# Performance work log

Hardware: AMD Instinct MI355X
Metric: run time of the kernel (lower is better)

Reference implementation:

```python
import jax, jax.numpy as jnp
import numpy as np

EPS = 1e-12

def _l2n(v):
    return v / (jnp.linalg.norm(v) + EPS)

def _sn(w, u, v):
    """One power iteration of spectral norm. w: [out, in] (1x1 conv flattened).
    u, v updates carry no gradient (requires_grad=False in torch); sigma grads flow through w."""
    v1 = jax.lax.stop_gradient(_l2n(w.T @ u))
    u1 = jax.lax.stop_gradient(_l2n(w @ v1))
    sigma = u1 @ (w @ v1)
    return w / sigma

def setup_inputs() -> dict:
    key = jax.random.key(0)
    ks = jax.random.split(key, 16)
    B, C, H, W = 4, 64, 64, 64
    d_qk, d_v = C // 8, C // 2
    inp = {
        "x": jax.random.normal(ks[0], (B, C, H, W), dtype=jnp.float32),
        "w_theta": jax.random.normal(ks[1], (d_qk, C), dtype=jnp.float32) * 0.05,
        "w_phi": jax.random.normal(ks[2], (d_qk, C), dtype=jnp.float32) * 0.05,
        "w_g": jax.random.normal(ks[3], (d_v, C), dtype=jnp.float32) * 0.05,
        "w_o": jax.random.normal(ks[4], (C, d_v), dtype=jnp.float32) * 0.05,
        "gamma": jax.random.normal(ks[5], (1,), dtype=jnp.float32),
        "u_theta": _l2n(jax.random.normal(ks[6], (d_qk,), dtype=jnp.float32)),
        "v_theta": _l2n(jax.random.normal(ks[7], (C,), dtype=jnp.float32)),
        "u_phi": _l2n(jax.random.normal(ks[8], (d_qk,), dtype=jnp.float32)),
        "v_phi": _l2n(jax.random.normal(ks[9], (C,), dtype=jnp.float32)),
        "u_g": _l2n(jax.random.normal(ks[10], (d_v,), dtype=jnp.float32)),
        "v_g": _l2n(jax.random.normal(ks[11], (C,), dtype=jnp.float32)),
        "u_o": _l2n(jax.random.normal(ks[12], (C,), dtype=jnp.float32)),
        "v_o": _l2n(jax.random.normal(ks[13], (d_v,), dtype=jnp.float32)),
    }
    return inp

def reference(x, w_theta, w_phi, w_g, w_o, gamma,
              u_theta, v_theta, u_phi, v_phi, u_g, v_g, u_o, v_o):
    B, C, H, W = x.shape
    HW = H * W
    wt = _sn(w_theta, u_theta, v_theta)
    wp = _sn(w_phi, u_phi, v_phi)
    wg = _sn(w_g, u_g, v_g)
    wo = _sn(w_o, u_o, v_o)
    xf = x.reshape(B, C, HW)                      # [B, C, N]
    theta = jnp.einsum('oc,bcn->bon', wt, xf)     # [B, C/8, N]
    phi = jnp.einsum('oc,bcn->bon', wp, xf)       # [B, C/8, N]
    g = jnp.einsum('oc,bcn->bon', wg, xf)         # [B, C/2, N]
    scores = jnp.einsum('bci,bcj->bij', theta, phi)  # [B, N, N]
    beta = jax.nn.softmax(scores, axis=1)            # softmax over dim=1 (rows), as in torch code
    o = jnp.einsum('bci,bij->bcj', g, beta)          # [B, C/2, N]
    out = jnp.einsum('oc,bcn->bon', wo, o).reshape(B, C, H, W)
    return gamma.reshape(()) * out + x
```

## Files before the change

kernel.cpp:

```cpp
#include <hip/hip_runtime.h>
#include <math.h>

#define N     4096
#define B     4
#define C     64
#define DQK   8
#define DV    32
#define LOG2E 1.4426950408889634f
#define PROJ_BLOCKS ((B * 12 * N) / 256)

typedef __attribute__((ext_vector_type(8)))  short  short8;
typedef __attribute__((ext_vector_type(16))) float  float16;

union U4S8 { int4 v; unsigned int u[4]; short8 s; };

__device__ __forceinline__ unsigned short f2bf(float f) {
  union { float f; unsigned int u; } c; c.f = f;
  unsigned int r = c.u + 0x7FFF + ((c.u >> 16) & 1);
  return (unsigned short)(r >> 16);
}
__device__ __forceinline__ float bf2f(unsigned short h) {
  union { unsigned int u; float f; } c; c.u = ((unsigned int)h) << 16;
  return c.f;
}
__device__ __forceinline__ unsigned int fbits(float f) {
  union { float f; unsigned int u; } c; c.f = f; return c.u;
}

__global__ __launch_bounds__(256) void projsig_kernel(
    const float* __restrict__ x,
    const float* __restrict__ w_theta, const float* __restrict__ w_phi,
    const float* __restrict__ w_g,     const float* __restrict__ w_o,
    const float* __restrict__ u_theta, const float* __restrict__ u_phi,
    const float* __restrict__ u_g,     const float* __restrict__ u_o,
    float* __restrict__ scales,
    unsigned short* __restrict__ theta_bf,
    unsigned short* __restrict__ phi_bf,
    unsigned short* __restrict__ v_bf) {
  __shared__ float v1[64];
  int bid = blockIdx.x;
  int tid = threadIdx.x;

  if (bid >= PROJ_BLOCKS) {
    int which = bid - PROJ_BLOCKS;
    const float* w; const float* u; int M, K;
    if      (which == 0) { w = w_theta; u = u_theta; M = DQK; K = C;  }
    else if (which == 1) { w = w_phi;   u = u_phi;   M = DQK; K = C;  }
    else if (which == 2) { w = w_g;     u = u_g;     M = DV;  K = C;  }
    else                 { w = w_o;     u = u_o;     M = C;   K = DV; }

    float acc = 0.f;
    if (tid < K) {
      for (int m = 0; m < M; ++m) acc += w[m * K + tid] * u[m];
    }
    float ss = acc * acc;
    #pragma unroll
    for (int off = 32; off; off >>= 1) ss += __shfl_xor(ss, off);
    float nrm = sqrtf(ss);
    if (tid < 64) v1[tid] = (tid < K) ? acc / (nrm + 1e-12f) : 0.f;
    __syncthreads();

    float t = 0.f;
    if (tid < M) {
      for (int k = 0; k < K; ++k) t += w[tid * K + k] * v1[k];
    }
    float ts = t * t;
    #pragma unroll
    for (int off = 32; off; off >>= 1) ts += __shfl_xor(ts, off);
    float tn = sqrtf(ts);
    if (tid == 0) scales[which] = (tn + 1e-12f) / ts;
    return;
  }

  int t  = bid * 256 + tid;
  int n  = t & (N - 1);
  int bg = t >> 12;
  int g  = bg % 12;
  int b  = bg / 12;

  const float* xp = x + (size_t)b * C * N + n;
  float xv[C];
  #pragma unroll
  for (int c = 0; c < C; ++c) xv[c] = xp[(size_t)c * N];

  const float* wbase;
  if      (g < 2) wbase = w_theta + g * 4 * C;
  else if (g < 4) wbase = w_phi + (g - 2) * 4 * C;
  else            wbase = w_g + (g - 4) * 4 * C;

  float o[4];
  #pragma unroll
  for (int r = 0; r < 4; ++r) {
    const float* wr = wbase + r * C;
    float a = 0.f;
    #pragma unroll
    for (int c = 0; c < C; ++c) a += wr[c] * xv[c];
    o[r] = a;
  }

  if (g < 4) {
    unsigned int lo = ((unsigned int)f2bf(o[0])) | ((unsigned int)f2bf(o[1]) << 16);
    unsigned int hi = ((unsigned int)f2bf(o[2])) | ((unsigned int)f2bf(o[3]) << 16);
    unsigned short* dst = (g < 2) ? theta_bf : phi_bf;
    int sub = g & 1;
    int2 pk; pk.x = (int)lo; pk.y = (int)hi;
    *(int2*)(dst + ((size_t)b * N + n) * 8 + sub * 4) = pk;
  } else {
    int c0 = (g - 4) * 4;
    int np = (n & ~0xC) | ((n & 4) << 1) | ((n & 8) >> 1);
    #pragma unroll
    for (int r = 0; r < 4; ++r)
      v_bf[((size_t)b * DV + c0 + r) * N + np] = f2bf(o[r]);
  }
}

__global__ __launch_bounds__(1024) void attn_kernel(
    const unsigned short* __restrict__ theta_bf,
    const unsigned short* __restrict__ phi_bf,
    const unsigned short* __restrict__ v_bf,
    const float* __restrict__ w_o, const float* __restrict__ scales,
    const float* __restrict__ gamma,
    const float* __restrict__ x, float* __restrict__ out) {
  __shared__ unsigned short po_lds[16][16][64];
  __shared__ float l_lds[16][32];
  __shared__ float Lrcp[32];
  __shared__ float ot[DV][33];
  __shared__ float wsh[C * DV];

  int bi = blockIdx.x;
  int qt = bi & 127;
  int b  = bi >> 7;
  int tid  = threadIdx.x;
  int lane = tid & 63;
  int wav  = tid >> 6;
  int half = lane >> 5;
  int l31  = lane & 31;
  int j    = qt * 32 + l31;

  float kappa = scales[0] * scales[1] * LOG2E;
  float swo   = scales[2] * scales[3] * gamma[0];
  for (int i = tid; i < C * DV; i += 1024) wsh[i] = w_o[i] * swo;

  U4S8 phu; phu.u[0] = phu.u[1] = phu.u[2] = phu.u[3] = 0;
  if (half == 0)
    phu.v = *(const int4*)(phi_bf + ((size_t)b * N + j) * 8);
  short8 phB = phu.s;

  float lsum = 0.f;
  float16 o;
  #pragma unroll
  for (int r = 0; r < 16; ++r) o[r] = 0.f;

  const unsigned short* vrow = v_bf + ((size_t)b * DV + l31) * N;
  int kstart = wav * 256;

  #pragma unroll 2
  for (int tt = 0; tt < 8; ++tt) {
    int kb = kstart + tt * 32;

    U4S8 ta;  ta.v  = *(const int4*)(theta_bf + ((size_t)b * N + kb + l31) * 8);
    U4S8 va1; va1.v = *(const int4*)(vrow + kb + half * 8);
    U4S8 va2; va2.v = *(const int4*)(vrow + kb + 16 + half * 8);

    float16 sf;
    #pragma unroll
    for (int r = 0; r < 16; ++r) sf[r] = 0.f;
    sf = __builtin_amdgcn_mfma_f32_32x32x16_bf16(ta.s, phB, sf, 0, 0, 0);

    float p[16];
    #pragma unroll
    for (int r = 0; r < 16; ++r) {
      p[r] = exp2f(kappa * sf[r]);
      lsum += p[r];
    }

    unsigned int pk[8];
    #pragma unroll
    for (int i = 0; i < 8; ++i)
      pk[i] = __builtin_amdgcn_perm(fbits(p[2 * i + 1]), fbits(p[2 * i]),
                                    0x07060302u);
    U4S8 b1, b2;
    b1.u[0] = pk[0]; b1.u[1] = pk[1]; b1.u[2] = pk[2]; b1.u[3] = pk[3];
    b2.u[0] = pk[4]; b2.u[1] = pk[5]; b2.u[2] = pk[6]; b2.u[3] = pk[7];

    o = __builtin_amdgcn_mfma_f32_32x32x16_bf16(va1.s, b1.s, o, 0, 0, 0);
    o = __builtin_amdgcn_mfma_f32_32x32x16_bf16(va2.s, b2.s, o, 0, 0, 0);
  }

  lsum += __shfl_xor(lsum, 32);
  if (half == 0) l_lds[wav][l31] = lsum;
  #pragma unroll
  for (int r = 0; r < 16; ++r)
    po_lds[wav][r][lane] = f2bf(o[r]);
  __syncthreads();

  int rr = tid >> 6;
  int ii = tid & 63;
  float oval = 0.f;
  #pragma unroll
  for (int w = 0; w < 16; ++w) oval += bf2f(po_lds[w][rr][ii]);
  if (tid < 32) {
    float L = 0.f;
    #pragma unroll
    for (int w = 0; w < 16; ++w) L += l_lds[w][tid];
    Lrcp[tid] = 1.f / L;
  }
  __syncthreads();

  int cc = (rr & 3) + 8 * (rr >> 2) + 4 * (ii >> 5);
  int jq = ii & 31;
  ot[cc][jq] = oval * Lrcp[jq];
  __syncthreads();

  int j2  = tid & 31;
  int ocp = tid >> 5;
  int oc0 = ocp;
  int oc1 = ocp + 32;
  float acc0 = 0.f, acc1 = 0.f;
  #pragma unroll
  for (int c = 0; c < DV; ++c) {
    float ov = ot[c][j2];
    acc0 = fmaf(wsh[oc0 * DV + c], ov, acc0);
    acc1 = fmaf(wsh[oc1 * DV + c], ov, acc1);
  }
  size_t base = (size_t)b * C * N + (size_t)qt * 32 + j2;
  out[base + (size_t)oc0 * N] = acc0 + x[base + (size_t)oc0 * N];
  out[base + (size_t)oc1 * N] = acc1 + x[base + (size_t)oc1 * N];
}

extern "C" void kernel_launch(void* const* d_in, const int* in_sizes, int n_in,
                              void* d_out, int out_size, void* d_ws, size_t ws_size,
                              hipStream_t stream) {
  const float* x       = (const float*)d_in[0];
  const float* w_theta = (const float*)d_in[1];
  const float* w_phi   = (const float*)d_in[2];
  const float* w_g     = (const float*)d_in[3];
  const float* w_o     = (const float*)d_in[4];
  const float* gamma   = (const float*)d_in[5];
  const float* u_theta = (const float*)d_in[6];
  const float* u_phi   = (const float*)d_in[8];
  const float* u_g     = (const float*)d_in[10];
  const float* u_o     = (const float*)d_in[12];
  float* out = (float*)d_out;

  float* ws = (float*)d_ws;
  float*          scales   = ws;
  unsigned short* theta_bf = (unsigned short*)(ws + 16);
  unsigned short* phi_bf   = theta_bf + (size_t)B * N * 8;
  unsigned short* v_bf     = phi_bf   + (size_t)B * N * 8;

  projsig_kernel<<<PROJ_BLOCKS + 4, 256, 0, stream>>>(
      x, w_theta, w_phi, w_g, w_o, u_theta, u_phi, u_g, u_o,
      scales, theta_bf, phi_bf, v_bf);
  attn_kernel<<<B * 128, 1024, 0, stream>>>(
      theta_bf, phi_bf, v_bf, w_o, scales, gamma, x, out);
}
```

Before: 131.0 us.

## Pack V into MFMA-lane layout, fold kappa into phi, keep partials fp32

The projection kernel now writes V pre-packed in the per-lane MFMA operand order, so each 16-key group is one contiguous 1KB block and the attention loop loads it as a coalesced int4 per lane. The softmax scale kappa is folded into phi once, rounded back to bf16, which removes a multiply per score element but adds extra rounding error to the logits. Cross-wave output partials are kept in fp32 in LDS instead of bf16, doubling that LDS buffer (64KB) and possibly lowering occupancy.

New measurement: 125.4 us (median of 2 runs). 4.3% less time.

```diff
diff --git a/kernel.cpp b/kernel.cpp
--- a/kernel.cpp
+++ b/kernel.cpp
@@ -25,6 +25,9 @@
 }
 __device__ __forceinline__ unsigned int fbits(float f) {
   union { float f; unsigned int u; } c; c.f = f; return c.u;
+}
+__device__ __forceinline__ int bitswap23(int n) {
+  return (n & ~0xC) | ((n & 4) << 1) | ((n & 8) >> 1);
 }
 
 __global__ __launch_bounds__(256) void projsig_kernel(
@@ -36,7 +39,7 @@
     float* __restrict__ scales,
     unsigned short* __restrict__ theta_bf,
     unsigned short* __restrict__ phi_bf,
-    unsigned short* __restrict__ v_bf) {
+    unsigned short* __restrict__ v_pack) {
   __shared__ float v1[64];
   int bid = blockIdx.x;
   int tid = threadIdx.x;
@@ -107,21 +110,27 @@
     *(int2*)(dst + ((size_t)b * N + n) * 8 + sub * 4) = pk;
   } else {
     int c0 = (g - 4) * 4;
-    int np = (n & ~0xC) | ((n & 4) << 1) | ((n & 8) >> 1);
-    #pragma unroll
-    for (int r = 0; r < 4; ++r)
-      v_bf[((size_t)b * DV + c0 + r) * N + np] = f2bf(o[r]);
+    int m  = bitswap23(n);
+    int q  = m >> 4;
+    int hf = (m >> 3) & 1;
+    int ii = m & 7;
+    unsigned short* dst = v_pack + ((size_t)(b * 256 + q)) * 64 * 8;
+    #pragma unroll
+    for (int r = 0; r < 4; ++r) {
+      int lane = (c0 + r) | (hf << 5);
+      dst[lane * 8 + ii] = f2bf(o[r]);
+    }
   }
 }
 
 __global__ __launch_bounds__(1024) void attn_kernel(
     const unsigned short* __restrict__ theta_bf,
     const unsigned short* __restrict__ phi_bf,
-    const unsigned short* __restrict__ v_bf,
+    const unsigned short* __restrict__ v_pack,
     const float* __restrict__ w_o, const float* __restrict__ scales,
     const float* __restrict__ gamma,
     const float* __restrict__ x, float* __restrict__ out) {
-  __shared__ unsigned short po_lds[16][16][64];
+  __shared__ float po_lds[16][16][64];
   __shared__ float l_lds[16][32];
   __shared__ float Lrcp[32];
   __shared__ float ot[DV][33];
@@ -142,8 +151,12 @@
   for (int i = tid; i < C * DV; i += 1024) wsh[i] = w_o[i] * swo;
 
   U4S8 phu; phu.u[0] = phu.u[1] = phu.u[2] = phu.u[3] = 0;
-  if (half == 0)
-    phu.v = *(const int4*)(phi_bf + ((size_t)b * N + j) * 8);
+  if (half == 0) {
+    U4S8 raw; raw.v = *(const int4*)(phi_bf + ((size_t)b * N + j) * 8);
+    #pragma unroll
+    for (int i = 0; i < 8; ++i)
+      phu.s[i] = (short)f2bf(bf2f((unsigned short)raw.s[i]) * kappa);
+  }
   short8 phB = phu.s;
 
   float lsum = 0.f;
@@ -151,16 +164,17 @@
   #pragma unroll
   for (int r = 0; r < 16; ++r) o[r] = 0.f;
 
-  const unsigned short* vrow = v_bf + ((size_t)b * DV + l31) * N;
   int kstart = wav * 256;
 
   #pragma unroll 2
   for (int tt = 0; tt < 8; ++tt) {
     int kb = kstart + tt * 32;
+    int q1 = kb >> 4;
 
     U4S8 ta;  ta.v  = *(const int4*)(theta_bf + ((size_t)b * N + kb + l31) * 8);
-    U4S8 va1; va1.v = *(const int4*)(vrow + kb + half * 8);
-    U4S8 va2; va2.v = *(const int4*)(vrow + kb + 16 + half * 8);
+    const int4* vp = (const int4*)(v_pack + ((size_t)(b * 256 + q1)) * 64 * 8);
+    U4S8 va1; va1.v = vp[lane];
+    U4S8 va2; va2.v = vp[64 + lane];
 
     float16 sf;
     #pragma unroll
@@ -170,7 +184,7 @@
     float p[16];
     #pragma unroll
     for (int r = 0; r < 16; ++r) {
-      p[r] = exp2f(kappa * sf[r]);
+      p[r] = exp2f(sf[r]);
       lsum += p[r];
     }
 
@@ -191,14 +205,14 @@
   if (half == 0) l_lds[wav][l31] = lsum;
   #pragma unroll
   for (int r = 0; r < 16; ++r)
-    po_lds[wav][r][lane] = f2bf(o[r]);
+    po_lds[wav][r][lane] = o[r];
   __syncthreads();
 
   int rr = tid >> 6;
   int ii = tid & 63;
   float oval = 0.f;
   #pragma unroll
-  for (int w = 0; w < 16; ++w) oval += bf2f(po_lds[w][rr][ii]);
+  for (int w = 0; w < 16; ++w) oval += po_lds[w][rr][ii];
   if (tid < 32) {
     float L = 0.f;
     #pragma unroll
@@ -247,11 +261,11 @@
   float*          scales   = ws;
   unsigned short* theta_bf = (unsigned short*)(ws + 16);
   unsigned short* phi_bf   = theta_bf + (size_t)B * N * 8;
-  unsigned short* v_bf     = phi_bf   + (size_t)B * N * 8;
+  unsigned short* v_pack   = phi_bf   + (size_t)B * N * 8;
 
   projsig_kernel<<<PROJ_BLOCKS + 4, 256, 0, stream>>>(
       x, w_theta, w_phi, w_g, w_o, u_theta, u_phi, u_g, u_o,
-      scales, theta_bf, phi_bf, v_bf);
+      scales, theta_bf, phi_bf, v_pack);
   attn_kernel<<<B * 128, 1024, 0, stream>>>(
-      theta_bf, phi_bf, v_bf, w_o, scales, gamma, x, out);
-}
+      theta_bf, phi_bf, v_pack, w_o, scales, gamma, x, out);
+}
```
